# Performance work log

Measured on AMD Instinct MI355X. Metric: run time of the kernel, lower is better.

The kernel has to match this reference:

```python
import jax
import jax.numpy as jnp
import numpy as np
import math

B, FRAMES, TLEN, E = 16, 8192, 512, 256
DUR = FRAMES // TLEN  # frames per phone


def setup_inputs() -> dict:
    key = jax.random.key(0)
    ks = jax.random.split(key, 8)
    encoder_out = jax.random.normal(ks[0], (B, TLEN, E), dtype=jnp.float32)
    # consecutively-distinct phone ids so the aligner advances exactly once per phone
    text_phone = jnp.broadcast_to(jnp.arange(TLEN, dtype=jnp.int32) % 97 + 1, (B, TLEN))
    align_phone = jnp.repeat(text_phone, DUR, axis=1)  # [B, FRAMES]
    pitch = jax.random.normal(ks[1], (B, FRAMES, 1), dtype=jnp.float32)
    beats = jax.random.randint(ks[2], (B, FRAMES, 1), 0, 2, dtype=jnp.int32)
    s = 1.0 / math.sqrt(E)
    fc_pitch_w = jax.random.normal(ks[3], (E, 1), dtype=jnp.float32)
    fc_pitch_b = jax.random.normal(ks[4], (E,), dtype=jnp.float32) * 0.01
    fc_pos_w = jax.random.normal(ks[5], (E, E), dtype=jnp.float32) * s
    fc_pos_b = jax.random.normal(ks[6], (E,), dtype=jnp.float32) * 0.01
    emb_beats = jax.random.normal(ks[7], (2, E), dtype=jnp.float32)
    return {"encoder_out": encoder_out, "align_phone": align_phone,
            "text_phone": text_phone, "pitch": pitch, "beats": beats,
            "fc_pitch_w": fc_pitch_w, "fc_pitch_b": fc_pitch_b,
            "fc_pos_w": fc_pos_w, "fc_pos_b": fc_pos_b, "emb_beats": emb_beats}


def _align_indices(ap, tp):
    """Replicates the eager aligner: ind_j = ind_{j-1} + (ap[j] != tp[ind_{j-1}]).
    ap: [FRAMES] int, tp: [TLEN] int -> [FRAMES] int32 gather indices."""
    tlen = tp.shape[0]

    def step(ind, a):
        new_ind = jnp.where(a == tp[ind], ind, jnp.minimum(ind + 1, tlen - 1))
        return new_ind, new_ind

    _, inds = jax.lax.scan(step, jnp.int32(0), ap[1:])
    return jnp.concatenate([jnp.zeros((1,), jnp.int32), inds])


def _positional_encoding(frames, d_model, dtype=jnp.float32):
    pos = jnp.arange(frames, dtype=jnp.float32)[:, None]            # [F,1]
    div = jnp.exp(jnp.arange(0, d_model, 2, dtype=jnp.float32) * (-math.log(10000.0) / d_model))
    pe = jnp.zeros((frames, d_model), dtype=jnp.float32)
    pe = pe.at[:, 0::2].set(jnp.sin(pos * div))
    pe = pe.at[:, 1::2].set(jnp.cos(pos * div))
    return pe.astype(dtype)


def reference(encoder_out, align_phone, text_phone, pitch, beats,
              fc_pitch_w, fc_pitch_b, fc_pos_w, fc_pos_b, emb_beats):
    # duration regulator: gather encoder states per frame  -> [B, FRAMES, E]
    inds = jax.vmap(_align_indices)(align_phone, text_phone)           # [B, FRAMES]
    aligner_out = jnp.take_along_axis(encoder_out, inds[..., None], axis=1)
    # pitch linear (in_features=1)
    pitch_proj = jnp.einsum('bfo,eo->bfe', pitch, fc_pitch_w) + fc_pitch_b
    # beats embedding
    beat_emb = emb_beats[beats[..., 0]]                                # [B, FRAMES, E]
    # positional encoding + fc_pos (PE added to aligner_out, dropout = identity)
    pe = _positional_encoding(aligner_out.shape[1], aligner_out.shape[2],
                              aligner_out.dtype)                        # [FRAMES, E]
    pos_out = jnp.einsum('bfe,de->bfd', aligner_out + pe[None], fc_pos_w) + fc_pos_b
    return aligner_out + pitch_proj + beat_emb + pos_out
```

## Files before the change

kernel.cpp:

```cpp
#include <hip/hip_runtime.h>
#include <hip/hip_bf16.h>

#define BATCH 16
#define FRAMES 8192
#define TLEN 512
#define EDIM 256
#define SP 56

typedef __attribute__((ext_vector_type(8))) short short8;
typedef __attribute__((ext_vector_type(4))) float f32x4;

__device__ __forceinline__ unsigned short f2bf(float f) {
    unsigned u = __float_as_uint(f);
    u = (u + 0x7fffu + ((u >> 16) & 1u)) >> 16;
    return (unsigned short)u;
}

__global__ __launch_bounds__(512) void k_prep(const float* __restrict__ X,
                                              const float* __restrict__ W,
                                              const float* __restrict__ pos_b,
                                              const float* __restrict__ pit_b,
                                              const int* __restrict__ ap,
                                              const int* __restrict__ tp,
                                              float* __restrict__ G,
                                              float* __restrict__ Q,
                                              int* __restrict__ inds) {
    __shared__ short lds[(64 + 256) * SP];
    int bid = blockIdx.x;
    int tid = threadIdx.x;

    if (bid >= 256) {
        int b = bid - 256;
        int* tps = (int*)lds;
        int* wsum = tps + TLEN;
        int* okp = wsum + 8;
        const int* apb = ap + b * FRAMES;
        tps[tid] = tp[b * TLEN + tid];
        if (tid == 0) *okp = 1;
        int j0 = tid * 16;
        int4 v0 = ((const int4*)apb)[tid * 4];
        int4 v1 = ((const int4*)apb)[tid * 4 + 1];
        int4 v2 = ((const int4*)apb)[tid * 4 + 2];
        int4 v3 = ((const int4*)apb)[tid * 4 + 3];
        int a[16] = {v0.x, v0.y, v0.z, v0.w, v1.x, v1.y, v1.z, v1.w,
                     v2.x, v2.y, v2.z, v2.w, v3.x, v3.y, v3.z, v3.w};
        int pr = (tid == 0) ? a[0] : apb[j0 - 1];
        int c = 0, p[16];
#pragma unroll
        for (int k = 0; k < 16; ++k) {
            c += ((j0 + k) > 0) && (a[k] != pr);
            p[k] = c;
            pr = a[k];
        }
        int lane = tid & 63, wv = tid >> 6;
        int sc = c;
#pragma unroll
        for (int d = 1; d < 64; d <<= 1) {
            int o = __shfl_up(sc, d);
            if (lane >= d) sc += o;
        }
        if (lane == 63) wsum[wv] = sc;
        __syncthreads();
        int wbase = 0;
        for (int w = 0; w < wv; ++w) wbase += wsum[w];
        int excl = wbase + sc - c;
        int g[16];
#pragma unroll
        for (int k = 0; k < 16; ++k) g[k] = min(excl + p[k], TLEN - 1);
        int4* ob = (int4*)(inds + b * FRAMES);
#pragma unroll
        for (int q4 = 0; q4 < 4; ++q4) {
            int4 wv4;
            wv4.x = g[q4 * 4]; wv4.y = g[q4 * 4 + 1];
            wv4.z = g[q4 * 4 + 2]; wv4.w = g[q4 * 4 + 3];
            ob[tid * 4 + q4] = wv4;
        }
        int ok = 1, gp = min(excl, TLEN - 1);
#pragma unroll
        for (int k = 0; k < 16; ++k) {
            int j = j0 + k, e;
            if (j == 0) e = 0;
            else e = (a[k] == tps[gp]) ? gp : min(gp + 1, TLEN - 1);
            ok &= (g[k] == e);
            gp = g[k];
        }
        if (!ok) atomicAnd(okp, 0);
        __syncthreads();
        if (*okp == 0 && tid == 0) {
            int ind = 0, cur = tps[0];
            int* o = inds + b * FRAMES;
            o[0] = 0;
            for (int j = 1; j < FRAMES; ++j) {
                int aj = apb[j];
                if (aj != cur && ind < TLEN - 1) { ind++; cur = tps[ind]; }
                o[j] = ind;
            }
        }
        return;
    }

    int qmode = (bid >= 128);
    int row0 = (qmode ? bid - 128 : bid) * 64;
    short* Xs = lds;
    short* Ws = lds + 64 * SP;
    int lane = tid & 63, wv = tid >> 6;
    int c = lane & 15, gq = lane >> 4;
    int r0 = (wv & 3) * 16, c0 = (wv >> 2) * 128;
    int sr = tid >> 3, spart = tid & 7;
    f32x4 acc[8];
#pragma unroll
    for (int i = 0; i < 8; ++i) acc[i] = (f32x4){0.f, 0.f, 0.f, 0.f};

    const float kPE = -0.03597789207803197f;
    const float INV2PI = 0.15915494309189535f;

    for (int ks = 0; ks < 8; ++ks) {
        int k0 = ks * 32;
        __syncthreads();
        {
            unsigned long long pk;
            if (!qmode) {
                f32x4 u = *(const f32x4*)(X + (row0 + sr) * EDIM + k0 + spart * 4);
                pk = (unsigned long long)f2bf(u[0]) |
                     ((unsigned long long)f2bf(u[1]) << 16) |
                     ((unsigned long long)f2bf(u[2]) << 32) |
                     ((unsigned long long)f2bf(u[3]) << 48);
            } else {
                float fr = (float)(row0 + sr);
                int i2 = (k0 + spart * 4) >> 1;
                float s0, c0f, s1, c1f;
                {
                    float dv = __expf((float)(2 * i2) * kPE);
                    float rev = fr * dv * INV2PI;
                    rev = rev - floorf(rev);
                    s0 = __builtin_amdgcn_sinf(rev);
                    c0f = __builtin_amdgcn_cosf(rev);
                }
                {
                    float dv = __expf((float)(2 * i2 + 2) * kPE);
                    float rev = fr * dv * INV2PI;
                    rev = rev - floorf(rev);
                    s1 = __builtin_amdgcn_sinf(rev);
                    c1f = __builtin_amdgcn_cosf(rev);
                }
                pk = (unsigned long long)f2bf(s0) |
                     ((unsigned long long)f2bf(c0f) << 16) |
                     ((unsigned long long)f2bf(s1) << 32) |
                     ((unsigned long long)f2bf(c1f) << 48);
            }
            *((unsigned long long*)&Xs[sr * SP + spart * 4]) = pk;
        }
#pragma unroll
        for (int m = 0; m < 4; ++m) {
            int d = sr + 64 * m;
            f32x4 u = *(const f32x4*)(W + d * EDIM + k0 + spart * 4);
            unsigned long long pk = (unsigned long long)f2bf(u[0]) |
                                    ((unsigned long long)f2bf(u[1]) << 16) |
                                    ((unsigned long long)f2bf(u[2]) << 32) |
                                    ((unsigned long long)f2bf(u[3]) << 48);
            *((unsigned long long*)&Ws[d * SP + spart * 4]) = pk;
        }
        __syncthreads();
        short8 afrag = *((const short8*)&Xs[(r0 + c) * SP + gq * 8]);
#pragma unroll
        for (int tc = 0; tc < 8; ++tc) {
            short8 bfrag = *((const short8*)&Ws[(c0 + tc * 16 + c) * SP + gq * 8]);
            acc[tc] = __builtin_amdgcn_mfma_f32_16x16x32_bf16(afrag, bfrag, acc[tc], 0, 0, 0);
        }
    }
    int mrow = row0 + r0 + gq * 4;
    if (!qmode) {
#pragma unroll
        for (int tc = 0; tc < 8; ++tc) {
            int d = c0 + tc * 16 + c;
#pragma unroll
            for (int i = 0; i < 4; ++i)
                G[(mrow + i) * EDIM + d] = acc[tc][i] + X[(mrow + i) * EDIM + d];
        }
    } else {
#pragma unroll
        for (int tc = 0; tc < 8; ++tc) {
            int d = c0 + tc * 16 + c;
            float bb = pos_b[d] + pit_b[d];
#pragma unroll
            for (int i = 0; i < 4; ++i)
                Q[(mrow + i) * EDIM + d] = acc[tc][i] + bb;
        }
    }
}

__global__ __launch_bounds__(256) void k_final(const float* __restrict__ G,
                                               const float* __restrict__ Q,
                                               const int* __restrict__ inds,
                                               const float* __restrict__ pitch,
                                               const int* __restrict__ beats,
                                               const float* __restrict__ wp,
                                               const float* __restrict__ eb,
                                               float* __restrict__ out) {
    int f = blockIdx.x * 4 + (threadIdx.x >> 6);
    int lane = threadIdx.x & 63;
    f32x4 q = ((const f32x4*)Q)[f * 64 + lane];
    f32x4 w4 = ((const f32x4*)wp)[lane];
    f32x4 e0 = ((const f32x4*)eb)[lane];
    f32x4 e1 = ((const f32x4*)eb)[64 + lane];
#pragma unroll
    for (int b = 0; b < BATCH; ++b) {
        int ind = inds[b * FRAMES + f];
        float p = pitch[b * FRAMES + f];
        int bt = beats[b * FRAMES + f];
        f32x4 g = ((const f32x4*)G)[(b * TLEN + ind) * 64 + lane];
        f32x4 e = bt ? e1 : e0;
        f32x4 r;
#pragma unroll
        for (int i = 0; i < 4; ++i) r[i] = g[i] + q[i] + p * w4[i] + e[i];
        __builtin_nontemporal_store(r, &((f32x4*)out)[(b * FRAMES + f) * 64 + lane]);
    }
}

extern "C" void kernel_launch(void* const* d_in, const int* in_sizes, int n_in,
                              void* d_out, int out_size, void* d_ws, size_t ws_size,
                              hipStream_t stream) {
    const float* enc   = (const float*)d_in[0];
    const int*   ap    = (const int*)d_in[1];
    const int*   tp    = (const int*)d_in[2];
    const float* pitch = (const float*)d_in[3];
    const int*   beats = (const int*)d_in[4];
    const float* wpit  = (const float*)d_in[5];
    const float* bpit  = (const float*)d_in[6];
    const float* wpos  = (const float*)d_in[7];
    const float* bpos  = (const float*)d_in[8];
    const float* ebts  = (const float*)d_in[9];
    float* out = (float*)d_out;
    char* ws = (char*)d_ws;
    int*   inds = (int*)ws;
    float* G    = (float*)(ws + (1 << 20));
    float* Q    = (float*)(ws + (9 << 20));

    hipLaunchKernelGGL(k_prep, dim3(272), dim3(512), 0, stream,
                       enc, wpos, bpos, bpit, ap, tp, G, Q, inds);
    hipLaunchKernelGGL(k_final, dim3(FRAMES / 4), dim3(256), 0, stream,
                       G, Q, inds, pitch, beats, wpit, ebts, out);
}
```

Measured before the change: 50.35 us.

## Fold identity into weight tile and remap final kernel to frame-batch tiles

The prep GEMM now adds 1.0 to the diagonal of the bf16 weight tile, so G = X·(W+I) comes straight from the accumulator and the epilogue no longer re-reads X. This makes the residual term bf16-rounded, which adds precision error. The final kernel now has each block cover 8 frames with 4 waves of 4 batches each, and uses a swizzled block order with a smaller grid. This changes the access pattern and gather locality across batches. A few pieces are refactored into a pack helper.

Result: faster. 45.79 us (-9.0%).

```diff
diff --git a/kernel.cpp b/kernel.cpp
--- a/kernel.cpp
+++ b/kernel.cpp
@@ -14,6 +14,12 @@
     unsigned u = __float_as_uint(f);
     u = (u + 0x7fffu + ((u >> 16) & 1u)) >> 16;
     return (unsigned short)u;
+}
+__device__ __forceinline__ unsigned long long pack4(f32x4 u) {
+    return (unsigned long long)f2bf(u[0]) |
+           ((unsigned long long)f2bf(u[1]) << 16) |
+           ((unsigned long long)f2bf(u[2]) << 32) |
+           ((unsigned long long)f2bf(u[3]) << 48);
 }
 
 __global__ __launch_bounds__(512) void k_prep(const float* __restrict__ X,
@@ -105,7 +111,7 @@
     short* Ws = lds + 64 * SP;
     int lane = tid & 63, wv = tid >> 6;
     int c = lane & 15, gq = lane >> 4;
-    int r0 = (wv & 3) * 16, c0 = (wv >> 2) * 128;
+    int r0 = (wv & 3) * 16, cc0 = (wv >> 2) * 128;
     int sr = tid >> 3, spart = tid & 7;
     f32x4 acc[8];
 #pragma unroll
@@ -121,32 +127,20 @@
             unsigned long long pk;
             if (!qmode) {
                 f32x4 u = *(const f32x4*)(X + (row0 + sr) * EDIM + k0 + spart * 4);
-                pk = (unsigned long long)f2bf(u[0]) |
-                     ((unsigned long long)f2bf(u[1]) << 16) |
-                     ((unsigned long long)f2bf(u[2]) << 32) |
-                     ((unsigned long long)f2bf(u[3]) << 48);
+                pk = pack4(u);
             } else {
                 float fr = (float)(row0 + sr);
-                int i2 = (k0 + spart * 4) >> 1;
-                float s0, c0f, s1, c1f;
-                {
-                    float dv = __expf((float)(2 * i2) * kPE);
-                    float rev = fr * dv * INV2PI;
-                    rev = rev - floorf(rev);
-                    s0 = __builtin_amdgcn_sinf(rev);
-                    c0f = __builtin_amdgcn_cosf(rev);
-                }
-                {
-                    float dv = __expf((float)(2 * i2 + 2) * kPE);
-                    float rev = fr * dv * INV2PI;
-                    rev = rev - floorf(rev);
-                    s1 = __builtin_amdgcn_sinf(rev);
-                    c1f = __builtin_amdgcn_cosf(rev);
-                }
-                pk = (unsigned long long)f2bf(s0) |
-                     ((unsigned long long)f2bf(c0f) << 16) |
-                     ((unsigned long long)f2bf(s1) << 32) |
-                     ((unsigned long long)f2bf(c1f) << 48);
+                int e0 = k0 + spart * 4;
+                float dv0 = __expf((float)e0 * kPE);
+                float dv1 = __expf((float)(e0 + 2) * kPE);
+                float a0 = fr * dv0 * INV2PI; a0 -= floorf(a0);
+                float a1 = fr * dv1 * INV2PI; a1 -= floorf(a1);
+                f32x4 v;
+                v[0] = __builtin_amdgcn_sinf(a0);
+                v[1] = __builtin_amdgcn_cosf(a0);
+                v[2] = __builtin_amdgcn_sinf(a1);
+                v[3] = __builtin_amdgcn_cosf(a1);
+                pk = pack4(v);
             }
             *((unsigned long long*)&Xs[sr * SP + spart * 4]) = pk;
         }
@@ -154,33 +148,34 @@
         for (int m = 0; m < 4; ++m) {
             int d = sr + 64 * m;
             f32x4 u = *(const f32x4*)(W + d * EDIM + k0 + spart * 4);
-            unsigned long long pk = (unsigned long long)f2bf(u[0]) |
-                                    ((unsigned long long)f2bf(u[1]) << 16) |
-                                    ((unsigned long long)f2bf(u[2]) << 32) |
-                                    ((unsigned long long)f2bf(u[3]) << 48);
-            *((unsigned long long*)&Ws[d * SP + spart * 4]) = pk;
-        }
-        __syncthreads();
-        short8 afrag = *((const short8*)&Xs[(r0 + c) * SP + gq * 8]);
+            if (!qmode) {
+#pragma unroll
+                for (int j = 0; j < 4; ++j)
+                    if (d == k0 + spart * 4 + j) u[j] += 1.0f;
+            }
+            *((unsigned long long*)&Ws[d * SP + spart * 4]) = pack4(u);
+        }
+        __syncthreads();
+        short8 af = *((const short8*)&Xs[(r0 + c) * SP + gq * 8]);
 #pragma unroll
         for (int tc = 0; tc < 8; ++tc) {
-            short8 bfrag = *((const short8*)&Ws[(c0 + tc * 16 + c) * SP + gq * 8]);
-            acc[tc] = __builtin_amdgcn_mfma_f32_16x16x32_bf16(afrag, bfrag, acc[tc], 0, 0, 0);
+            short8 bf = *((const short8*)&Ws[(cc0 + tc * 16 + c) * SP + gq * 8]);
+            acc[tc] = __builtin_amdgcn_mfma_f32_16x16x32_bf16(af, bf, acc[tc], 0, 0, 0);
         }
     }
     int mrow = row0 + r0 + gq * 4;
     if (!qmode) {
 #pragma unroll
         for (int tc = 0; tc < 8; ++tc) {
-            int d = c0 + tc * 16 + c;
+            int d = cc0 + tc * 16 + c;
 #pragma unroll
             for (int i = 0; i < 4; ++i)
-                G[(mrow + i) * EDIM + d] = acc[tc][i] + X[(mrow + i) * EDIM + d];
+                G[(mrow + i) * EDIM + d] = acc[tc][i];
         }
     } else {
 #pragma unroll
         for (int tc = 0; tc < 8; ++tc) {
-            int d = c0 + tc * 16 + c;
+            int d = cc0 + tc * 16 + c;
             float bb = pos_b[d] + pit_b[d];
 #pragma unroll
             for (int i = 0; i < 4; ++i)
@@ -197,23 +192,29 @@
                                                const float* __restrict__ wp,
                                                const float* __restrict__ eb,
                                                float* __restrict__ out) {
-    int f = blockIdx.x * 4 + (threadIdx.x >> 6);
-    int lane = threadIdx.x & 63;
-    f32x4 q = ((const f32x4*)Q)[f * 64 + lane];
+    int swz = (blockIdx.x & 7) * 128 + (blockIdx.x >> 3);
+    int f0 = swz * 8;
+    int wv = threadIdx.x >> 6, lane = threadIdx.x & 63;
     f32x4 w4 = ((const f32x4*)wp)[lane];
     f32x4 e0 = ((const f32x4*)eb)[lane];
     f32x4 e1 = ((const f32x4*)eb)[64 + lane];
 #pragma unroll
-    for (int b = 0; b < BATCH; ++b) {
-        int ind = inds[b * FRAMES + f];
-        float p = pitch[b * FRAMES + f];
-        int bt = beats[b * FRAMES + f];
-        f32x4 g = ((const f32x4*)G)[(b * TLEN + ind) * 64 + lane];
-        f32x4 e = bt ? e1 : e0;
-        f32x4 r;
-#pragma unroll
-        for (int i = 0; i < 4; ++i) r[i] = g[i] + q[i] + p * w4[i] + e[i];
-        __builtin_nontemporal_store(r, &((f32x4*)out)[(b * FRAMES + f) * 64 + lane]);
+    for (int f = 0; f < 8; ++f) {
+        f32x4 q = ((const f32x4*)Q)[(f0 + f) * 64 + lane];
+#pragma unroll
+        for (int bb = 0; bb < 4; ++bb) {
+            int b = wv * 4 + bb;
+            int idx = b * FRAMES + f0 + f;
+            int ind = inds[idx];
+            float p = pitch[idx];
+            int bt = beats[idx];
+            f32x4 g = ((const f32x4*)G)[(b * TLEN + ind) * 64 + lane];
+            f32x4 e = bt ? e1 : e0;
+            f32x4 r;
+#pragma unroll
+            for (int i = 0; i < 4; ++i) r[i] = g[i] + q[i] + p * w4[i] + e[i];
+            __builtin_nontemporal_store(r, &((f32x4*)out)[idx * 64 + lane]);
+        }
     }
 }
 
@@ -238,6 +239,6 @@
 
     hipLaunchKernelGGL(k_prep, dim3(272), dim3(512), 0, stream,
                        enc, wpos, bpos, bpit, ap, tp, G, Q, inds);
-    hipLaunchKernelGGL(k_final, dim3(FRAMES / 4), dim3(256), 0, stream,
+    hipLaunchKernelGGL(k_final, dim3(1024), dim3(256), 0, stream,
                        G, Q, inds, pitch, beats, wpit, ebts, out);
 }
```
